# Kernel tuning notes

Measured on AMD Instinct MI355X. Metric: run time of the kernel, lower is better.

## Reference

```python
import jax, jax.numpy as jnp
import numpy as np

N = 50000      # n_nodes
E = 800000     # edges (before self-loops)
IN = 128       # in_dim
HID = 32       # hidden_dim (per-head out channels)
HEADS = 4
EMB = 128      # embed_dim
LAYERS = 3
NEG_SLOPE = 0.2  # PyG GATv2 default leaky_relu slope


def _layer_norm(x, g, b):
    mu = jnp.mean(x, axis=-1, keepdims=True)
    var = jnp.var(x, axis=-1, keepdims=True)
    return g * (x - mu) / jnp.sqrt(var + 1e-5) + b


def _gatv2(h, src, dst, n, Wl, bl, Wr, br, att, bias):
    # GATv2Conv (PyG semantics, share_weights=False, concat=True).
    H, C = att.shape
    xl = (h @ Wl + bl).reshape(n, H, C)   # target (i) transform
    xr = (h @ Wr + br).reshape(n, H, C)   # source (j) transform
    x_i = xl[dst]                          # [Etot, H, C] gather
    x_j = xr[src]
    e = jax.nn.leaky_relu(x_i + x_j, NEG_SLOPE)
    logit = jnp.einsum('ehc,hc->eh', e, att)          # [Etot, H]
    # segment softmax over destination node (every node has a self-loop)
    m = jax.ops.segment_max(logit, dst, num_segments=n)
    ex = jnp.exp(logit - m[dst])
    den = jax.ops.segment_sum(ex, dst, num_segments=n)
    alpha = ex / (den[dst] + 1e-16)
    out = jax.ops.segment_sum(alpha[..., None] * x_j, dst, num_segments=n)
    return out.reshape(n, H * C) + bias


def setup_inputs() -> dict:
    key = jax.random.key(0)
    ks = iter(jax.random.split(key, 64))
    d = {}
    d['x'] = jax.random.normal(next(ks), (N, IN), jnp.float32)
    d['edge_index'] = jax.random.randint(next(ks), (2, E), 0, N, dtype=jnp.int64)

    def w(shape, fan):
        return jax.random.normal(next(ks), shape, jnp.float32) / np.float32(np.sqrt(fan))

    HC = HID * HEADS
    d['W_in'] = w((IN, HID), IN); d['b_in'] = jnp.zeros((HID,), jnp.float32)
    for i in range(LAYERS):
        ic = HID if i == 0 else HC
        d[f'Wl{i}'] = w((ic, HC), ic); d[f'bl{i}'] = jnp.zeros((HC,), jnp.float32)
        d[f'Wr{i}'] = w((ic, HC), ic); d[f'br{i}'] = jnp.zeros((HC,), jnp.float32)
        d[f'att{i}'] = w((HEADS, HID), HID)
        d[f'bo{i}'] = jnp.zeros((HC,), jnp.float32)
        d[f'g{i}'] = jnp.ones((HC,), jnp.float32)
        d[f'be{i}'] = jnp.zeros((HC,), jnp.float32)
    d['W_out'] = w((HC, EMB), HC); d['b_out'] = jnp.zeros((EMB,), jnp.float32)
    return d


def reference(x, edge_index, W_in, b_in,
              Wl0, bl0, Wr0, br0, att0, bo0, g0, be0,
              Wl1, bl1, Wr1, br1, att1, bo1, g1, be1,
              Wl2, bl2, Wr2, br2, att2, bo2, g2, be2,
              W_out, b_out):
    n = x.shape[0]
    loops = jnp.arange(n, dtype=edge_index.dtype)  # add_self_loops=True
    src = jnp.concatenate([edge_index[0], loops])
    dst = jnp.concatenate([edge_index[1], loops])

    h = jax.nn.gelu(x @ W_in + b_in, approximate=False)
    layers = [(Wl0, bl0, Wr0, br0, att0, bo0, g0, be0),
              (Wl1, bl1, Wr1, br1, att1, bo1, g1, be1),
              (Wl2, bl2, Wr2, br2, att2, bo2, g2, be2)]
    for (Wl, bl, Wr, br, att, bo, g, be) in layers:
        h_new = jax.nn.gelu(_layer_norm(_gatv2(h, src, dst, n, Wl, bl, Wr, br, att, bo), g, be), approximate=False)
        h = h + h_new if h.shape == h_new.shape else h_new  # dropout = identity (eval)
    out = h @ W_out + b_out
    norm = jnp.maximum(jnp.linalg.norm(out, axis=-1, keepdims=True), 1e-12)
    return out / norm
```

## Files before the change

kernel.cpp:

```cpp
#include <hip/hip_runtime.h>
#include <hip/hip_bf16.h>
#include <math.h>

#define N_NODES 50000
#define N_EDGES 800000
#define IN_DIM  128
#define HC_DIM  128
#define HID_C   32
#define SCAN_NB 196

typedef __attribute__((ext_vector_type(8))) short short8;
typedef __attribute__((ext_vector_type(4))) short short4v;
typedef __attribute__((ext_vector_type(4))) float f32x4;

__device__ __forceinline__ float gelu_f(float x){
    return 0.5f*x*(1.0f + erff(x*0.7071067811865475f));
}

__device__ __forceinline__ void split2(float f, short& h, short& l){
    __hip_bfloat16 bh = __float2bfloat16(f);
    float r = f - __bfloat162float(bh);
    __hip_bfloat16 blo = __float2bfloat16(r);
    h = *reinterpret_cast<short*>(&bh);
    l = *reinterpret_cast<short*>(&blo);
}
__device__ __forceinline__ unsigned short f2bf(float f){
    __hip_bfloat16 b = __float2bfloat16(f);
    return *reinterpret_cast<unsigned short*>(&b);
}
__device__ __forceinline__ float bf2f(unsigned short u){
    return __uint_as_float(((unsigned)u)<<16);
}

__global__ __launch_bounds__(256) void k_count(const int* __restrict__ dst, int* __restrict__ cnt){
    int e = blockIdx.x*256 + threadIdx.x;
    if(e<N_EDGES) atomicAdd(&cnt[dst[e]], 1);
}

__global__ __launch_bounds__(256) void k_scan1(const int* __restrict__ cnt, int* __restrict__ rowptr,
                                               int* __restrict__ part){
    __shared__ int sh[256];
    int t=threadIdx.x; int i=blockIdx.x*256+t;
    int v = (i<N_NODES)? cnt[i] : 0;
    sh[t]=v; __syncthreads();
    for(int off=1; off<256; off<<=1){
        int y = (t>=off)? sh[t-off] : 0;
        __syncthreads();
        sh[t] += y;
        __syncthreads();
    }
    if(i<N_NODES) rowptr[i] = sh[t]-v;
    if(t==255) part[blockIdx.x] = sh[255];
}

__global__ __launch_bounds__(256) void k_scan2(int* __restrict__ part){
    __shared__ int sh[256];
    int t=threadIdx.x;
    int v = (t<SCAN_NB)? part[t] : 0;
    sh[t]=v; __syncthreads();
    for(int off=1; off<256; off<<=1){
        int y=(t>=off)? sh[t-off]:0;
        __syncthreads();
        sh[t]+=y;
        __syncthreads();
    }
    if(t<SCAN_NB) part[t] = sh[t]-v;
}

__global__ __launch_bounds__(256) void k_scan3(int* __restrict__ rowptr, const int* __restrict__ part,
                                               int* __restrict__ cur){
    int t=threadIdx.x; int i=blockIdx.x*256+t;
    if(i<N_NODES){
        int v = rowptr[i] + part[blockIdx.x];
        rowptr[i]=v; cur[i]=v;
    }
    if(i==0) rowptr[N_NODES]=N_EDGES;
}

__global__ __launch_bounds__(256) void k_fill(const int* __restrict__ src, const int* __restrict__ dst,
                                              int* __restrict__ cur, int* __restrict__ col){
    int e = blockIdx.x*256+threadIdx.x;
    if(e<N_EDGES){
        int d = dst[e];
        int p = atomicAdd(&cur[d],1);
        col[p] = src[e];
    }
}

__global__ __launch_bounds__(256) void k_splitW(const float* __restrict__ W0, const float* __restrict__ W1,
                                                const float* __restrict__ W2, const float* __restrict__ W3,
                                                const float* __restrict__ W4, const float* __restrict__ W5,
                                                const float* __restrict__ W6, short* __restrict__ WT){
    int bx = blockIdx.x;
    int m, kc;
    if(bx < 2){ m = bx; kc = 0; }
    else { m = 2 + (bx-2)/4; kc = (bx-2)&3; }
    const float* src; int K; size_t off;
    switch(m){
        case 0: src=W0; K=32;  off=0;      break;
        case 1: src=W1; K=32;  off=8192;   break;
        case 2: src=W2; K=128; off=16384;  break;
        case 3: src=W3; K=128; off=49152;  break;
        case 4: src=W4; K=128; off=81920;  break;
        case 5: src=W5; K=128; off=114688; break;
        default:src=W6; K=128; off=147456; break;
    }
    short* hi = WT + off;
    short* lo = hi + (size_t)K*HC_DIM;
    #pragma unroll
    for(int i=0;i<16;i++){
        int idx = threadIdx.x + i*256;
        int k = kc*32 + (idx>>7);
        int n = idx & 127;
        float f = src[(size_t)k*HC_DIM + n];
        short h,l; split2(f,h,l);
        hi[(size_t)n*K + k] = h;
        lo[(size_t)n*K + k] = l;
    }
}

__global__ __launch_bounds__(256) void k_gemm_in(const float* __restrict__ x, const float* __restrict__ W,
                                                 const float* __restrict__ b, float* __restrict__ h,
                                                 short* __restrict__ hhi, short* __restrict__ hlo){
    int id = blockIdx.x*256+threadIdx.x;
    int r = id>>5, c = id&31;
    const float4* x4 = (const float4*)(x + (size_t)r*IN_DIM);
    float acc=0.f;
    #pragma unroll 8
    for(int k=0;k<IN_DIM/4;k++){
        float4 xv = x4[k];
        acc = fmaf(xv.x, W[(4*k  )*HID_C+c], acc);
        acc = fmaf(xv.y, W[(4*k+1)*HID_C+c], acc);
        acc = fmaf(xv.z, W[(4*k+2)*HID_C+c], acc);
        acc = fmaf(xv.w, W[(4*k+3)*HID_C+c], acc);
    }
    float v = gelu_f(acc + b[c]);
    h[(size_t)r*HID_C+c] = v;
    short hh,ll; split2(v,hh,ll);
    hhi[(size_t)r*HID_C+c] = hh;
    hlo[(size_t)r*HID_C+c] = ll;
}

template<int K, bool PAIR, bool NORM>
__global__ __launch_bounds__(256) void k_mfma(const short* __restrict__ Ahi, const short* __restrict__ Alo,
                                              const short* __restrict__ WTl, const float* __restrict__ bl,
                                              const short* __restrict__ WTr, const float* __restrict__ br,
                                              float* __restrict__ XL, unsigned short* __restrict__ XR16){
    constexpr int LDS_K = 40;
    constexpr int NCH = K / 32;
    __shared__ short As_hi[64*LDS_K], As_lo[64*LDS_K];
    __shared__ short Bh0[128*LDS_K], Bl0[128*LDS_K];
    __shared__ short Bh1[PAIR?128*LDS_K:1], Bl1[PAIR?128*LDS_K:1];
    __shared__ float ssq[NORM?256:1];

    int t = threadIdx.x;
    int lane = t & 63, wave = t >> 6;
    int quad = lane >> 4, ml = lane & 15;
    int rbase = blockIdx.x * 64;

    const short* WTl_lo = WTl + (size_t)K*HC_DIM;
    const short* WTr_lo = PAIR ? (WTr + (size_t)K*HC_DIM) : nullptr;

    f32x4 accL[4][2], accR[4][2];
    #pragma unroll
    for(int i=0;i<4;i++)
        #pragma unroll
        for(int j=0;j<2;j++){ accL[i][j]=(f32x4){0,0,0,0}; accR[i][j]=(f32x4){0,0,0,0}; }

    int r = t >> 2, seg = t & 3;
    int gr = rbase + r; if(gr >= N_NODES) gr = N_NODES-1;

    for(int c=0; c<NCH; c++){
        if(c) __syncthreads();
        size_t ka = (size_t)gr*K + c*32 + seg*8;
        *(short8*)(As_hi + r*LDS_K + seg*8) = *(const short8*)(Ahi + ka);
        *(short8*)(As_lo + r*LDS_K + seg*8) = *(const short8*)(Alo + ka);
        #pragma unroll
        for(int u=0; u<2; u++){
            int uu = t + u*256;
            int n = uu >> 2, sg = uu & 3;
            size_t kw = (size_t)n*K + c*32 + sg*8;
            *(short8*)(Bh0 + n*LDS_K + sg*8) = *(const short8*)(WTl + kw);
            *(short8*)(Bl0 + n*LDS_K + sg*8) = *(const short8*)(WTl_lo + kw);
            if(PAIR){
                *(short8*)(Bh1 + n*LDS_K + sg*8) = *(const short8*)(WTr + kw);
                *(short8*)(Bl1 + n*LDS_K + sg*8) = *(const short8*)(WTr_lo + kw);
            }
        }
        __syncthreads();

        int k0 = quad*8;
        short8 ah[4], al[4];
        #pragma unroll
        for(int i=0;i<4;i++){
            ah[i] = *(const short8*)(As_hi + (16*i + ml)*LDS_K + k0);
            al[i] = *(const short8*)(As_lo + (16*i + ml)*LDS_K + k0);
        }
        #pragma unroll
        for(int j=0;j<2;j++){
            int nrow = j*64 + wave*16 + ml;
            short8 bh = *(const short8*)(Bh0 + nrow*LDS_K + k0);
            short8 blo = *(const short8*)(Bl0 + nrow*LDS_K + k0);
            #pragma unroll
            for(int i=0;i<4;i++){
                accL[i][j] = __builtin_amdgcn_mfma_f32_16x16x32_bf16(ah[i], bh,  accL[i][j], 0,0,0);
                accL[i][j] = __builtin_amdgcn_mfma_f32_16x16x32_bf16(ah[i], blo, accL[i][j], 0,0,0);
                accL[i][j] = __builtin_amdgcn_mfma_f32_16x16x32_bf16(al[i], bh,  accL[i][j], 0,0,0);
            }
            if(PAIR){
                short8 ch = *(const short8*)(Bh1 + nrow*LDS_K + k0);
                short8 cl = *(const short8*)(Bl1 + nrow*LDS_K + k0);
                #pragma unroll
                for(int i=0;i<4;i++){
                    accR[i][j] = __builtin_amdgcn_mfma_f32_16x16x32_bf16(ah[i], ch, accR[i][j], 0,0,0);
                    accR[i][j] = __builtin_amdgcn_mfma_f32_16x16x32_bf16(ah[i], cl, accR[i][j], 0,0,0);
                    accR[i][j] = __builtin_amdgcn_mfma_f32_16x16x32_bf16(al[i], ch, accR[i][j], 0,0,0);
                }
            }
        }
    }

    int col0 = wave*16 + ml, col1 = 64 + wave*16 + ml;
    float bL0 = bl[col0], bL1 = bl[col1];

    if(NORM){
        #pragma unroll
        for(int i=0;i<4;i++){
            #pragma unroll
            for(int rr=0;rr<4;rr++){
                float v0 = accL[i][0][rr] + bL0;
                float v1 = accL[i][1][rr] + bL1;
                float p = v0*v0 + v1*v1;
                p += __shfl_xor(p,1); p += __shfl_xor(p,2);
                p += __shfl_xor(p,4); p += __shfl_xor(p,8);
                if(ml==0) ssq[wave*64 + 16*i + quad*4 + rr] = p;
            }
        }
        __syncthreads();
        #pragma unroll
        for(int i=0;i<4;i++){
            #pragma unroll
            for(int rr=0;rr<4;rr++){
                int row = 16*i + quad*4 + rr;
                int grr = rbase + row;
                if(grr < N_NODES){
                    float tot = ssq[row] + ssq[64+row] + ssq[128+row] + ssq[192+row];
                    float inv = 1.0f / fmaxf(sqrtf(tot), 1e-12f);
                    XL[(size_t)grr*HC_DIM + col0] = (accL[i][0][rr] + bL0) * inv;
                    XL[(size_t)grr*HC_DIM + col1] = (accL[i][1][rr] + bL1) * inv;
                }
            }
        }
    } else {
        float bR0 = PAIR ? br[col0] : 0.f, bR1 = PAIR ? br[col1] : 0.f;
        #pragma unroll
        for(int i=0;i<4;i++){
            #pragma unroll
            for(int rr=0;rr<4;rr++){
                int grr = rbase + 16*i + quad*4 + rr;
                if(grr < N_NODES){
                    XL[(size_t)grr*HC_DIM + col0] = accL[i][0][rr] + bL0;
                    XL[(size_t)grr*HC_DIM + col1] = accL[i][1][rr] + bL1;
                    if(PAIR){
                        XR16[(size_t)grr*HC_DIM + col0] = f2bf(accR[i][0][rr] + bR0);
                        XR16[(size_t)grr*HC_DIM + col1] = f2bf(accR[i][1][rr] + bR1);
                    }
                }
            }
        }
    }
}

__global__ __launch_bounds__(256) void k_node(const float* __restrict__ XL, const unsigned short* __restrict__ XR,
    const int* __restrict__ rowptr, const int* __restrict__ colidx,
    const float* __restrict__ att, const float* __restrict__ bo,
    const float* __restrict__ gg, const float* __restrict__ be,
    const float* __restrict__ hold, float* __restrict__ hout,
    short* __restrict__ hi_out, short* __restrict__ lo_out)
{
    int wave=threadIdx.x>>6, lane=threadIdx.x&63;
    int node = blockIdx.x*4+wave;
    int cg = lane & 31, half = lane >> 5;
    int c4 = cg << 2;

    float4 xl = *(const float4*)(XL + (size_t)node*HC_DIM + c4);
    float4 av = *(const float4*)(att + c4);
    int beg = rowptr[node], end = rowptr[node+1];

    #define LOADX(j, xx) { ushort4 u_ = *(const ushort4*)(XR + (size_t)(j)*HC_DIM + c4); \
        xx = make_float4(bf2f(u_.x), bf2f(u_.y), bf2f(u_.z), bf2f(u_.w)); }
    #define EDGE_LOGIT(xj, q) { \
        float u0 = xl.x + xj.x; u0 = (u0>0.f)?u0:0.2f*u0; \
        float u1 = xl.y + xj.y; u1 = (u1>0.f)?u1:0.2f*u1; \
        float u2 = xl.z + xj.z; u2 = (u2>0.f)?u2:0.2f*u2; \
        float u3 = xl.w + xj.w; u3 = (u3>0.f)?u3:0.2f*u3; \
        q = fmaf(u0,av.x, fmaf(u1,av.y, fmaf(u2,av.z, u3*av.w))); \
        q += __shfl_xor(q,1); q += __shfl_xor(q,2); q += __shfl_xor(q,4); }

    float4 xs; LOADX(node, xs)
    float qs; EDGE_LOGIT(xs, qs)
    float m, ls; float4 acc;
    if(half==0){ m = qs; ls = 1.f; acc = xs; }
    else       { m = -INFINITY; ls = 0.f; acc = make_float4(0.f,0.f,0.f,0.f); }

    int P = end - beg;
    int nb = P >> 3;
    int base = beg;
    for(int b=0; b<nb; b++, base += 8){
        int j0 = colidx[base     + half];
        int j1 = colidx[base + 2 + half];
        int j2 = colidx[base + 4 + half];
        int j3 = colidx[base + 6 + half];
        float4 x0, x1, x2, x3;
        LOADX(j0, x0) LOADX(j1, x1) LOADX(j2, x2) LOADX(j3, x3)
        float q0,q1,q2,q3;
        EDGE_LOGIT(x0,q0) EDGE_LOGIT(x1,q1) EDGE_LOGIT(x2,q2) EDGE_LOGIT(x3,q3)
        float nm = fmaxf(m, fmaxf(fmaxf(q0,q1),fmaxf(q2,q3)));
        float sc = __expf(m-nm);
        float e0 = __expf(q0-nm), e1 = __expf(q1-nm);
        float e2 = __expf(q2-nm), e3 = __expf(q3-nm);
        ls = fmaf(ls, sc, (e0+e1)+(e2+e3));
        acc.x = fmaf(acc.x, sc, fmaf(e0,x0.x, fmaf(e1,x1.x, fmaf(e2,x2.x, e3*x3.x))));
        acc.y = fmaf(acc.y, sc, fmaf(e0,x0.y, fmaf(e1,x1.y, fmaf(e2,x2.y, e3*x3.y))));
        acc.z = fmaf(acc.z, sc, fmaf(e0,x0.z, fmaf(e1,x1.z, fmaf(e2,x2.z, e3*x3.z))));
        acc.w = fmaf(acc.w, sc, fmaf(e0,x0.w, fmaf(e1,x1.w, fmaf(e2,x2.w, e3*x3.w))));
        m = nm;
    }
    #pragma unroll
    for(int i=0;i<4;i++){
        int idx = base + 2*i + half;
        if(idx < end){
            int j = colidx[idx];
            float4 xj; LOADX(j, xj)
            float q; EDGE_LOGIT(xj, q)
            float nm = fmaxf(m, q);
            float sc = __expf(m-nm);
            float p  = __expf(q-nm);
            ls = fmaf(ls, sc, p);
            acc.x = fmaf(acc.x, sc, p*xj.x);
            acc.y = fmaf(acc.y, sc, p*xj.y);
            acc.z = fmaf(acc.z, sc, p*xj.z);
            acc.w = fmaf(acc.w, sc, p*xj.w);
            m = nm;
        }
    }
    #undef EDGE_LOGIT
    #undef LOADX

    {
        float mo  = __shfl_xor(m, 32);
        float lso = __shfl_xor(ls, 32);
        float4 ao;
        ao.x = __shfl_xor(acc.x,32); ao.y = __shfl_xor(acc.y,32);
        ao.z = __shfl_xor(acc.z,32); ao.w = __shfl_xor(acc.w,32);
        float nm = fmaxf(m, mo);
        float s0 = __expf(m-nm), s1 = __expf(mo-nm);
        ls = ls*s0 + lso*s1;
        acc.x = acc.x*s0 + ao.x*s1;
        acc.y = acc.y*s0 + ao.y*s1;
        acc.z = acc.z*s0 + ao.z*s1;
        acc.w = acc.w*s0 + ao.w*s1;
    }

    float inv = 1.0f/ls;
    float4 bo4 = *(const float4*)(bo + c4);
    float o0 = fmaf(acc.x,inv,bo4.x), o1 = fmaf(acc.y,inv,bo4.y);
    float o2 = fmaf(acc.z,inv,bo4.z), o3 = fmaf(acc.w,inv,bo4.w);
    float s1v = (o0+o1)+(o2+o3);
    float s2v = fmaf(o0,o0, fmaf(o1,o1, fmaf(o2,o2, o3*o3)));
    #pragma unroll
    for(int msk=1;msk<32;msk<<=1){ s1v += __shfl_xor(s1v,msk); s2v += __shfl_xor(s2v,msk); }
    float mean = s1v*(1.f/128.f);
    float var  = s2v*(1.f/128.f) - mean*mean;
    float rstd = rsqrtf(var + 1e-5f);
    float4 g4  = *(const float4*)(gg + c4);
    float4 be4 = *(const float4*)(be + c4);
    float r0 = gelu_f(fmaf(g4.x*(o0-mean), rstd, be4.x));
    float r1 = gelu_f(fmaf(g4.y*(o1-mean), rstd, be4.y));
    float r2 = gelu_f(fmaf(g4.z*(o2-mean), rstd, be4.z));
    float r3 = gelu_f(fmaf(g4.w*(o3-mean), rstd, be4.w));
    if(hold){
        float4 hv = *(const float4*)(hold + (size_t)node*HC_DIM + c4);
        r0 += hv.x; r1 += hv.y; r2 += hv.z; r3 += hv.w;
    }
    if(half==0){
        *(float4*)(hout + (size_t)node*HC_DIM + c4) = make_float4(r0,r1,r2,r3);
        short4v vh, vl; short hh, ll;
        split2(r0,hh,ll); vh[0]=hh; vl[0]=ll;
        split2(r1,hh,ll); vh[1]=hh; vl[1]=ll;
        split2(r2,hh,ll); vh[2]=hh; vl[2]=ll;
        split2(r3,hh,ll); vh[3]=hh; vl[3]=ll;
        *(short4v*)(hi_out + (size_t)node*HC_DIM + c4) = vh;
        *(short4v*)(lo_out + (size_t)node*HC_DIM + c4) = vl;
    }
}

extern "C" void kernel_launch(void* const* d_in, const int* in_sizes, int n_in,
                              void* d_out, int out_size, void* d_ws, size_t ws_size,
                              hipStream_t stream)
{
    const float* x   = (const float*)d_in[0];
    const int*   ei  = (const int*)  d_in[1];
    const float* Win = (const float*)d_in[2];
    const float* bin = (const float*)d_in[3];
    const float *Wl[3], *bl[3], *Wr[3], *br[3], *att[3], *bo[3], *gg[3], *be[3];
    for(int i=0;i<3;i++){
        const int base = 4 + 8*i;
        Wl[i]=(const float*)d_in[base+0]; bl[i]=(const float*)d_in[base+1];
        Wr[i]=(const float*)d_in[base+2]; br[i]=(const float*)d_in[base+3];
        att[i]=(const float*)d_in[base+4]; bo[i]=(const float*)d_in[base+5];
        gg[i]=(const float*)d_in[base+6]; be[i]=(const float*)d_in[base+7];
    }
    const float* Wout=(const float*)d_in[28];
    const float* bout=(const float*)d_in[29];
    float* out = (float*)d_out;

    char* w = (char*)d_ws;
    float* hA = (float*)w;  w += (size_t)N_NODES*HC_DIM*4;
    float* hB = (float*)w;  w += (size_t)N_NODES*HC_DIM*4;
    float* XL = (float*)w;  w += (size_t)N_NODES*HC_DIM*4;
    unsigned short* XR16 = (unsigned short*)w; w += (size_t)N_NODES*HC_DIM*2;
    short* hAhi = (short*)w; w += (size_t)N_NODES*HC_DIM*2;
    short* hAlo = (short*)w; w += (size_t)N_NODES*HC_DIM*2;
    short* hBhi = (short*)w; w += (size_t)N_NODES*HC_DIM*2;
    short* hBlo = (short*)w; w += (size_t)N_NODES*HC_DIM*2;
    short* WT   = (short*)w; w += (size_t)180224*2;
    int* rowptr = (int*)w;  w += (size_t)(N_NODES+2)*4;
    int* cursor = (int*)w;  w += (size_t)N_NODES*4;
    int* colidx = (int*)w;  w += (size_t)N_EDGES*4;
    int* part   = (int*)w;  w += 256*4;

    const int* srcp = ei;
    const int* dstp = ei + N_EDGES;

    const short* WTl0 = WT + 0;      const short* WTr0 = WT + 8192;
    const short* WTl1 = WT + 16384;  const short* WTr1 = WT + 49152;
    const short* WTl2 = WT + 81920;  const short* WTr2 = WT + 114688;
    const short* WTo  = WT + 147456;

    k_splitW<<<22,256,0,stream>>>(Wl[0],Wr[0],Wl[1],Wr[1],Wl[2],Wr[2],Wout, WT);
    hipMemsetAsync(cursor, 0, (size_t)N_NODES*4, stream);
    k_count <<<3125,256, 0, stream>>>(dstp, cursor);
    k_scan1 <<<SCAN_NB,256,0,stream>>>(cursor, rowptr, part);
    k_scan2 <<<1,   256, 0, stream>>>(part);
    k_scan3 <<<SCAN_NB,256,0,stream>>>(rowptr, part, cursor);
    k_fill  <<<3125,256, 0, stream>>>(srcp, dstp, cursor, colidx);
    k_gemm_in<<<6250,256,0,stream>>>(x, Win, bin, hA, hAhi, hAlo);

    k_mfma<32,true,false><<<782,256,0,stream>>>(hAhi, hAlo, WTl0, bl[0], WTr0, br[0], XL, XR16);
    k_node<<<12500,256,0,stream>>>(XL,XR16,rowptr,colidx,att[0],bo[0],gg[0],be[0],
                                   (const float*)nullptr, hB, hBhi, hBlo);

    k_mfma<128,true,false><<<782,256,0,stream>>>(hBhi, hBlo, WTl1, bl[1], WTr1, br[1], XL, XR16);
    k_node<<<12500,256,0,stream>>>(XL,XR16,rowptr,colidx,att[1],bo[1],gg[1],be[1], hB, hA, hAhi, hAlo);

    k_mfma<128,true,false><<<782,256,0,stream>>>(hAhi, hAlo, WTl2, bl[2], WTr2, br[2], XL, XR16);
    k_node<<<12500,256,0,stream>>>(XL,XR16,rowptr,colidx,att[2],bo[2],gg[2],be[2], hA, hB, hBhi, hBlo);

    k_mfma<128,false,true><<<782,256,0,stream>>>(hBhi, hBlo, WTo, bout, nullptr, nullptr, out, nullptr);
}
```

Baseline: 515.9 us.

## Record atomic ranks in count pass, batch node tail, and use exp2 softmax

The count kernel now saves each edge's atomic slot rank, so the fill kernel writes col[rowptr[dst]+rank] directly instead of running a second atomic pass over the cursor array. Both kernels process four edges per thread. In the node aggregation kernel, att is pre-scaled by log2(e) so the softmax can use exp2f, leaky ReLU becomes a fmaxf, and the serial per-edge tail loop is replaced by one batched 4-edge step that masks unused slots to -inf. This trades an extra rank buffer of one int per edge for fewer atomics, and the tail batch does redundant loads of the node's own row for padded slots.

```diff
diff --git a/kernel.cpp b/kernel.cpp
--- a/kernel.cpp
+++ b/kernel.cpp
@@ -8,6 +8,7 @@
 #define HC_DIM  128
 #define HID_C   32
 #define SCAN_NB 196
+#define LOG2E   1.4426950408889634f
 
 typedef __attribute__((ext_vector_type(8))) short short8;
 typedef __attribute__((ext_vector_type(4))) short short4v;
@@ -32,9 +33,14 @@
     return __uint_as_float(((unsigned)u)<<16);
 }
 
-__global__ __launch_bounds__(256) void k_count(const int* __restrict__ dst, int* __restrict__ cnt){
-    int e = blockIdx.x*256 + threadIdx.x;
-    if(e<N_EDGES) atomicAdd(&cnt[dst[e]], 1);
+__global__ __launch_bounds__(256) void k_count(const int* __restrict__ dst, int* __restrict__ cnt,
+                                               int* __restrict__ rank){
+    int b = blockIdx.x*1024 + threadIdx.x;
+    #pragma unroll
+    for(int i=0;i<4;i++){
+        int e = b + i*256;
+        if(e < N_EDGES) rank[e] = atomicAdd(&cnt[dst[e]], 1);
+    }
 }
 
 __global__ __launch_bounds__(256) void k_scan1(const int* __restrict__ cnt, int* __restrict__ rowptr,
@@ -67,23 +73,20 @@
     if(t<SCAN_NB) part[t] = sh[t]-v;
 }
 
-__global__ __launch_bounds__(256) void k_scan3(int* __restrict__ rowptr, const int* __restrict__ part,
-                                               int* __restrict__ cur){
+__global__ __launch_bounds__(256) void k_scan3(int* __restrict__ rowptr, const int* __restrict__ part){
     int t=threadIdx.x; int i=blockIdx.x*256+t;
-    if(i<N_NODES){
-        int v = rowptr[i] + part[blockIdx.x];
-        rowptr[i]=v; cur[i]=v;
-    }
+    if(i<N_NODES) rowptr[i] += part[blockIdx.x];
     if(i==0) rowptr[N_NODES]=N_EDGES;
 }
 
 __global__ __launch_bounds__(256) void k_fill(const int* __restrict__ src, const int* __restrict__ dst,
-                                              int* __restrict__ cur, int* __restrict__ col){
-    int e = blockIdx.x*256+threadIdx.x;
-    if(e<N_EDGES){
-        int d = dst[e];
-        int p = atomicAdd(&cur[d],1);
-        col[p] = src[e];
+                                              const int* __restrict__ rowptr, const int* __restrict__ rank,
+                                              int* __restrict__ col){
+    int b = blockIdx.x*1024 + threadIdx.x;
+    #pragma unroll
+    for(int i=0;i<4;i++){
+        int e = b + i*256;
+        if(e < N_EDGES) col[rowptr[dst[e]] + rank[e]] = src[e];
     }
 }
 
@@ -285,15 +288,16 @@
 
     float4 xl = *(const float4*)(XL + (size_t)node*HC_DIM + c4);
     float4 av = *(const float4*)(att + c4);
+    av.x *= LOG2E; av.y *= LOG2E; av.z *= LOG2E; av.w *= LOG2E;
     int beg = rowptr[node], end = rowptr[node+1];
 
     #define LOADX(j, xx) { ushort4 u_ = *(const ushort4*)(XR + (size_t)(j)*HC_DIM + c4); \
         xx = make_float4(bf2f(u_.x), bf2f(u_.y), bf2f(u_.z), bf2f(u_.w)); }
     #define EDGE_LOGIT(xj, q) { \
-        float u0 = xl.x + xj.x; u0 = (u0>0.f)?u0:0.2f*u0; \
-        float u1 = xl.y + xj.y; u1 = (u1>0.f)?u1:0.2f*u1; \
-        float u2 = xl.z + xj.z; u2 = (u2>0.f)?u2:0.2f*u2; \
-        float u3 = xl.w + xj.w; u3 = (u3>0.f)?u3:0.2f*u3; \
+        float u0 = xl.x + xj.x; u0 = fmaxf(u0, 0.2f*u0); \
+        float u1 = xl.y + xj.y; u1 = fmaxf(u1, 0.2f*u1); \
+        float u2 = xl.z + xj.z; u2 = fmaxf(u2, 0.2f*u2); \
+        float u3 = xl.w + xj.w; u3 = fmaxf(u3, 0.2f*u3); \
         q = fmaf(u0,av.x, fmaf(u1,av.y, fmaf(u2,av.z, u3*av.w))); \
         q += __shfl_xor(q,1); q += __shfl_xor(q,2); q += __shfl_xor(q,4); }
 
@@ -316,9 +320,9 @@
         float q0,q1,q2,q3;
         EDGE_LOGIT(x0,q0) EDGE_LOGIT(x1,q1) EDGE_LOGIT(x2,q2) EDGE_LOGIT(x3,q3)
         float nm = fmaxf(m, fmaxf(fmaxf(q0,q1),fmaxf(q2,q3)));
-        float sc = __expf(m-nm);
-        float e0 = __expf(q0-nm), e1 = __expf(q1-nm);
-        float e2 = __expf(q2-nm), e3 = __expf(q3-nm);
+        float sc = exp2f(m-nm);
+        float e0 = exp2f(q0-nm), e1 = exp2f(q1-nm);
+        float e2 = exp2f(q2-nm), e3 = exp2f(q3-nm);
         ls = fmaf(ls, sc, (e0+e1)+(e2+e3));
         acc.x = fmaf(acc.x, sc, fmaf(e0,x0.x, fmaf(e1,x1.x, fmaf(e2,x2.x, e3*x3.x))));
         acc.y = fmaf(acc.y, sc, fmaf(e0,x0.y, fmaf(e1,x1.y, fmaf(e2,x2.y, e3*x3.y))));
@@ -326,21 +330,29 @@
         acc.w = fmaf(acc.w, sc, fmaf(e0,x0.w, fmaf(e1,x1.w, fmaf(e2,x2.w, e3*x3.w))));
         m = nm;
     }
-    #pragma unroll
-    for(int i=0;i<4;i++){
-        int idx = base + 2*i + half;
-        if(idx < end){
-            int j = colidx[idx];
-            float4 xj; LOADX(j, xj)
-            float q; EDGE_LOGIT(xj, q)
-            float nm = fmaxf(m, q);
-            float sc = __expf(m-nm);
-            float p  = __expf(q-nm);
-            ls = fmaf(ls, sc, p);
-            acc.x = fmaf(acc.x, sc, p*xj.x);
-            acc.y = fmaf(acc.y, sc, p*xj.y);
-            acc.z = fmaf(acc.z, sc, p*xj.z);
-            acc.w = fmaf(acc.w, sc, p*xj.w);
+    if(base < end){
+        int i0 = base + half, i1 = base + 2 + half, i2 = base + 4 + half, i3 = base + 6 + half;
+        int j0 = (i0<end)? colidx[i0] : node;
+        int j1 = (i1<end)? colidx[i1] : node;
+        int j2 = (i2<end)? colidx[i2] : node;
+        int j3 = (i3<end)? colidx[i3] : node;
+        float4 x0, x1, x2, x3;
+        LOADX(j0, x0) LOADX(j1, x1) LOADX(j2, x2) LOADX(j3, x3)
+        float q0,q1,q2,q3;
+        EDGE_LOGIT(x0,q0) EDGE_LOGIT(x1,q1) EDGE_LOGIT(x2,q2) EDGE_LOGIT(x3,q3)
+        if(i1>=end) q1 = -INFINITY;
+        if(i2>=end) q2 = -INFINITY;
+        if(i3>=end) q3 = -INFINITY;
+        if(i0 < end){
+            float nm = fmaxf(m, fmaxf(fmaxf(q0,q1),fmaxf(q2,q3)));
+            float sc = exp2f(m-nm);
+            float e0 = exp2f(q0-nm), e1 = exp2f(q1-nm);
+            float e2 = exp2f(q2-nm), e3 = exp2f(q3-nm);
+            ls = fmaf(ls, sc, (e0+e1)+(e2+e3));
+            acc.x = fmaf(acc.x, sc, fmaf(e0,x0.x, fmaf(e1,x1.x, fmaf(e2,x2.x, e3*x3.x))));
+            acc.y = fmaf(acc.y, sc, fmaf(e0,x0.y, fmaf(e1,x1.y, fmaf(e2,x2.y, e3*x3.y))));
+            acc.z = fmaf(acc.z, sc, fmaf(e0,x0.z, fmaf(e1,x1.z, fmaf(e2,x2.z, e3*x3.z))));
+            acc.w = fmaf(acc.w, sc, fmaf(e0,x0.w, fmaf(e1,x1.w, fmaf(e2,x2.w, e3*x3.w))));
             m = nm;
         }
     }
@@ -354,7 +366,7 @@
         ao.x = __shfl_xor(acc.x,32); ao.y = __shfl_xor(acc.y,32);
         ao.z = __shfl_xor(acc.z,32); ao.w = __shfl_xor(acc.w,32);
         float nm = fmaxf(m, mo);
-        float s0 = __expf(m-nm), s1 = __expf(mo-nm);
+        float s0 = exp2f(m-nm), s1 = exp2f(mo-nm);
         ls = ls*s0 + lso*s1;
         acc.x = acc.x*s0 + ao.x*s1;
         acc.y = acc.y*s0 + ao.y*s1;
@@ -428,6 +440,7 @@
     int* rowptr = (int*)w;  w += (size_t)(N_NODES+2)*4;
     int* cursor = (int*)w;  w += (size_t)N_NODES*4;
     int* colidx = (int*)w;  w += (size_t)N_EDGES*4;
+    int* rank   = (int*)w;  w += (size_t)N_EDGES*4;
     int* part   = (int*)w;  w += 256*4;
 
     const int* srcp = ei;
@@ -440,11 +453,11 @@
 
     k_splitW<<<22,256,0,stream>>>(Wl[0],Wr[0],Wl[1],Wr[1],Wl[2],Wr[2],Wout, WT);
     hipMemsetAsync(cursor, 0, (size_t)N_NODES*4, stream);
-    k_count <<<3125,256, 0, stream>>>(dstp, cursor);
+    k_count <<<782,256, 0, stream>>>(dstp, cursor, rank);
     k_scan1 <<<SCAN_NB,256,0,stream>>>(cursor, rowptr, part);
     k_scan2 <<<1,   256, 0, stream>>>(part);
-    k_scan3 <<<SCAN_NB,256,0,stream>>>(rowptr, part, cursor);
-    k_fill  <<<3125,256, 0, stream>>>(srcp, dstp, cursor, colidx);
+    k_scan3 <<<SCAN_NB,256,0,stream>>>(rowptr, part);
+    k_fill  <<<782,256, 0, stream>>>(srcp, dstp, rowptr, rank, colidx);
     k_gemm_in<<<6250,256,0,stream>>>(x, Win, bin, hA, hAhi, hAlo);
 
     k_mfma<32,true,false><<<782,256,0,stream>>>(hAhi, hAlo, WTl0, bl[0], WTr0, br[0], XL, XR16);
```

Result: faster. 500.3 us (-3.0%).
